# Performance work log

Hardware: AMD Instinct MI355X
Metric: run time of the kernel (lower is better)

## Reference

```python
import jax, jax.numpy as jnp
import numpy as np

TEXT_DIM, GIN = 5000, 128
B, N, E = 4096, 200000, 6400000
AE_HID, AE_EMB, G_HID, G_EMB = 8, 4, 8, 4


def _gcn(x, W, b, src, dst):
    N_ = x.shape[0]
    h = x @ W
    loop = jnp.arange(N_)
    s = jnp.concatenate([src, loop])
    d = jnp.concatenate([dst, loop])
    deg = jax.ops.segment_sum(jnp.ones(s.shape[0], h.dtype), d, num_segments=N_)
    dinv = jnp.where(deg > 0, jax.lax.rsqrt(jnp.maximum(deg, 1e-12)), 0.0)
    norm = dinv[s] * dinv[d]
    out = jax.ops.segment_sum(h[s] * norm[:, None], d, num_segments=N_)
    return out + b


def setup_inputs() -> dict:
    key = jax.random.key(0)
    ks = jax.random.split(key, 20)
    def lin(k, fan_in, fan_out):
        lim = 1.0 / np.sqrt(fan_in)
        kw, kb = jax.random.split(k)
        W = jax.random.uniform(kw, (fan_in, fan_out), jnp.float32, -lim, lim)
        b = jax.random.uniform(kb, (fan_out,), jnp.float32, -lim, lim)
        return W, b
    W_e1, b_e1 = lin(ks[0], TEXT_DIM, AE_HID)
    W_e2, b_e2 = lin(ks[1], AE_HID, AE_EMB)
    W_d1, b_d1 = lin(ks[2], AE_EMB, AE_HID)
    W_d2, b_d2 = lin(ks[3], AE_HID, TEXT_DIM)
    W_g1, b_g1 = lin(ks[4], GIN, G_HID)
    W_g2, b_g2 = lin(ks[5], G_HID, G_EMB)
    W_c, b_c = lin(ks[6], AE_EMB + G_EMB, 1)
    text_x = jax.random.normal(ks[7], (B, TEXT_DIM), jnp.float32)
    node_x = jax.random.normal(ks[8], (N, GIN), jnp.float32)
    edge_index = jax.random.randint(ks[9], (2, E), 0, N, jnp.int64 if jax.config.jax_enable_x64 else jnp.int32)
    batch = jnp.sort(jax.random.randint(ks[10], (N,), 0, B, edge_index.dtype))
    return {"text_x": text_x, "node_x": node_x, "edge_index": edge_index, "batch": batch,
            "W_e1": W_e1, "b_e1": b_e1, "W_e2": W_e2, "b_e2": b_e2,
            "W_d1": W_d1, "b_d1": b_d1, "W_d2": W_d2, "b_d2": b_d2,
            "W_g1": W_g1, "b_g1": b_g1, "W_g2": W_g2, "b_g2": b_g2,
            "W_c": W_c, "b_c": b_c}


def reference(text_x, node_x, edge_index, batch,
              W_e1, b_e1, W_e2, b_e2, W_d1, b_d1, W_d2, b_d2,
              W_g1, b_g1, W_g2, b_g2, W_c, b_c):
    # Autoencoder (eval mode: dropout = identity)
    z_text = jax.nn.relu(jax.nn.relu(text_x @ W_e1 + b_e1) @ W_e2 + b_e2)
    x_hat = jax.nn.sigmoid(jax.nn.relu(z_text @ W_d1 + b_d1) @ W_d2 + b_d2)
    # GNN encoder
    src, dst = edge_index[0], edge_index[1]
    h = jax.nn.relu(_gcn(node_x, W_g1, b_g1, src, dst))
    h = _gcn(h, W_g2, b_g2, src, dst)
    # global mean pool over graphs
    nb = text_x.shape[0]
    sums = jax.ops.segment_sum(h, batch, num_segments=nb)
    cnt = jax.ops.segment_sum(jnp.ones(h.shape[0], h.dtype), batch, num_segments=nb)
    z_graph = sums / jnp.maximum(cnt, 1.0)[:, None]
    z = jnp.concatenate([z_text, z_graph], axis=1)
    logits = z @ W_c + b_c
    return (x_hat, logits, z)
```

## Files before the change

kernel.cpp:

```cpp
#include <hip/hip_runtime.h>

#define BB 4096
#define TD 5000
#define NN 200000
#define EE 6400000
#define NBK 782

__device__ __forceinline__ void atomAddF(float* p, float v) {
    unsafeAtomicAdd(p, v);
}

__global__ void k_zero(float* p, int n) {
    int i = blockIdx.x * 256 + threadIdx.x;
    if (i < n) p[i] = 0.f;
}

__global__ void k_detect(const int* __restrict__ e, int* __restrict__ flag) {
    __shared__ int r[256];
    int tid = threadIdx.x;
    int acc = 0;
    for (int i = tid; i < 4096; i += 256) acc |= e[2 * i + 1];
    r[tid] = acc;
    __syncthreads();
    for (int s = 128; s > 0; s >>= 1) {
        if (tid < s) r[tid] |= r[tid + s];
        __syncthreads();
    }
    if (tid == 0) *flag = (r[0] == 0) ? 1 : 0;
}

__global__ void k_deg_init(unsigned int* deg) {
    int i = blockIdx.x * 256 + threadIdx.x;
    if (i < NN) deg[i] = 1u;
}

__global__ void k_rank(const int* __restrict__ edge, const int* __restrict__ flag,
                       unsigned int* __restrict__ deg, unsigned int* __restrict__ r) {
    int e = blockIdx.x * 256 + threadIdx.x;
    if (e >= EE) return;
    int f = *flag;
    int d = f ? edge[2 * (EE + e)] : edge[EE + e];
    r[e] = atomicAdd(&deg[d], 1u);
}

__global__ void k_dinv(const unsigned int* __restrict__ deg, float* __restrict__ dinv) {
    int i = blockIdx.x * 256 + threadIdx.x;
    if (i < NN) dinv[i] = rsqrtf((float)deg[i]);
}

__global__ void kA_blocksum(const unsigned int* __restrict__ deg, unsigned int* __restrict__ bsum) {
    __shared__ unsigned int s[256];
    int tid = threadIdx.x;
    int i = blockIdx.x * 256 + tid;
    s[tid] = (i < NN) ? (deg[i] - 1u) : 0u;
    __syncthreads();
    for (int st = 128; st > 0; st >>= 1) {
        if (tid < st) s[tid] += s[tid + st];
        __syncthreads();
    }
    if (tid == 0) bsum[blockIdx.x] = s[0];
}
__global__ void kB_scanblocks(const unsigned int* __restrict__ bsum, unsigned int* __restrict__ bpre,
                              unsigned int* __restrict__ indptr) {
    __shared__ unsigned int s[1024];
    int t = threadIdx.x;
    s[t] = (t < NBK) ? bsum[t] : 0u;
    __syncthreads();
    for (int off = 1; off < 1024; off <<= 1) {
        unsigned int v = (t >= off) ? s[t - off] : 0u;
        __syncthreads();
        s[t] += v;
        __syncthreads();
    }
    if (t < NBK) bpre[t] = (t == 0) ? 0u : s[t - 1];
    if (t == 0) indptr[NN] = EE;
}
__global__ void kC_indptr(const unsigned int* __restrict__ deg, const unsigned int* __restrict__ bpre,
                          unsigned int* __restrict__ indptr) {
    __shared__ unsigned int s[256];
    int tid = threadIdx.x;
    int i = blockIdx.x * 256 + tid;
    unsigned int c = (i < NN) ? (deg[i] - 1u) : 0u;
    s[tid] = c;
    __syncthreads();
    for (int off = 1; off < 256; off <<= 1) {
        unsigned int v = (tid >= off) ? s[tid - off] : 0u;
        __syncthreads();
        s[tid] += v;
        __syncthreads();
    }
    if (i < NN) indptr[i] = bpre[blockIdx.x] + s[tid] - c;
}

__global__ void k_place(const int* __restrict__ edge, const int* __restrict__ flag,
                        const unsigned int* __restrict__ indptr, const unsigned int* __restrict__ r,
                        int* __restrict__ csr_src) {
    int e = blockIdx.x * 256 + threadIdx.x;
    if (e >= EE) return;
    int f = *flag;
    int s = f ? edge[2 * e] : edge[e];
    int d = f ? edge[2 * (EE + e)] : edge[EE + e];
    csr_src[indptr[d] + r[e] - 1u] = s;
}

__global__ __launch_bounds__(256) void k_gcn1_mm(
    const float* __restrict__ nodex, const float* __restrict__ Wg1,
    const float* __restrict__ dinv, float* __restrict__ h0g)
{
    __shared__ float W[128 * 8];
    int tid = threadIdx.x;
    for (int i = tid; i < 1024; i += 256) W[i] = Wg1[i];
    __syncthreads();
    int row = blockIdx.x * 256 + tid;
    if (row >= NN) return;
    const float4* xr = (const float4*)(nodex + (size_t)row * 128);
    float acc[8];
#pragma unroll
    for (int j = 0; j < 8; j++) acc[j] = 0.f;
#pragma unroll 8
    for (int c = 0; c < 32; c++) {
        float4 v = xr[c];
        const float* wr = &W[c * 32];
#pragma unroll
        for (int j = 0; j < 8; j++)
            acc[j] += v.x * wr[j] + v.y * wr[8 + j] + v.z * wr[16 + j] + v.w * wr[24 + j];
    }
    float di = dinv[row];
    float* o = h0g + (size_t)row * 8;
#pragma unroll
    for (int j = 0; j < 8; j++) o[j] = di * acc[j];
}

__global__ __launch_bounds__(256) void k_gather1(
    const unsigned int* __restrict__ indptr, const int* __restrict__ csr_src,
    const float* __restrict__ h0g, const float* __restrict__ dinv,
    const float* __restrict__ bg1, const float* __restrict__ Wg2,
    float* __restrict__ h2g)
{
    __shared__ float W[32];
    __shared__ float b1[8];
    __shared__ float h1s[4][8];
    int tid = threadIdx.x;
    if (tid < 32) W[tid] = Wg2[tid];
    if (tid < 8) b1[tid] = bg1[tid];
    __syncthreads();
    int wid = tid >> 6, lane = tid & 63;
    int i = blockIdx.x * 4 + wid;
    if (i < NN) {
        int beg = indptr[i], end = indptr[i + 1];
        int f = lane & 7;
        float a = 0.f;
        for (int k = beg + (lane >> 3); k < end; k += 8)
            a += h0g[(size_t)csr_src[k] * 8 + f];
        a += __shfl_xor(a, 8, 64);
        a += __shfl_xor(a, 16, 64);
        a += __shfl_xor(a, 32, 64);
        if (lane < 8) {
            float di = dinv[i];
            h1s[wid][f] = fmaxf(di * (a + h0g[(size_t)i * 8 + f]) + b1[f], 0.f);
        }
    }
    __syncthreads();
    if (i < NN && lane < 4) {
        float di = dinv[i];
        float s = 0.f;
#pragma unroll
        for (int k = 0; k < 8; k++) s += h1s[wid][k] * W[k * 4 + lane];
        h2g[(size_t)i * 4 + lane] = di * s;
    }
}

__global__ __launch_bounds__(256) void k_gather2(
    const unsigned int* __restrict__ indptr, const int* __restrict__ csr_src,
    const float* __restrict__ h2g, const float* __restrict__ dinv,
    const float* __restrict__ bg2, const int* __restrict__ batch,
    const int* __restrict__ flag, float* __restrict__ pool, float* __restrict__ cnt)
{
    __shared__ float b2[4];
    int tid = threadIdx.x;
    if (tid < 4) b2[tid] = bg2[tid];
    __syncthreads();
    int wid = tid >> 6, lane = tid & 63;
    int i = blockIdx.x * 4 + wid;
    if (i >= NN) return;
    int beg = indptr[i], end = indptr[i + 1];
    int f = lane & 3;
    float a = 0.f;
    for (int k = beg + (lane >> 2); k < end; k += 16)
        a += h2g[(size_t)csr_src[k] * 4 + f];
    a += __shfl_xor(a, 4, 64);
    a += __shfl_xor(a, 8, 64);
    a += __shfl_xor(a, 16, 64);
    a += __shfl_xor(a, 32, 64);
    if (lane < 4) {
        float di = dinv[i];
        float h = di * (a + h2g[(size_t)i * 4 + f]) + b2[f];
        int fg = *flag;
        int b = fg ? batch[2 * i] : batch[i];
        atomAddF(&pool[(size_t)b * 4 + f], h);
        if (f == 0) atomAddF(&cnt[b], 1.f);
    }
}

__global__ __launch_bounds__(256) void k_ae_encode(
    const float* __restrict__ text,
    const float* __restrict__ We1, const float* __restrict__ be1,
    const float* __restrict__ We2, const float* __restrict__ be2,
    float* __restrict__ z_text)
{
    __shared__ float red[8][256];
    __shared__ float t1[8];
    int row = blockIdx.x, tid = threadIdx.x;
    const float* xrow = text + (size_t)row * TD;
    float acc[8];
#pragma unroll
    for (int j = 0; j < 8; j++) acc[j] = 0.f;
    for (int i = tid; i < TD; i += 256) {
        float x = xrow[i];
        const float* wr = We1 + (size_t)i * 8;
#pragma unroll
        for (int j = 0; j < 8; j++) acc[j] += x * wr[j];
    }
#pragma unroll
    for (int j = 0; j < 8; j++) red[j][tid] = acc[j];
    __syncthreads();
    for (int s = 128; s > 0; s >>= 1) {
        if (tid < s) {
#pragma unroll
            for (int j = 0; j < 8; j++) red[j][tid] += red[j][tid + s];
        }
        __syncthreads();
    }
    if (tid < 8) t1[tid] = fmaxf(red[tid][0] + be1[tid], 0.f);
    __syncthreads();
    if (tid < 4) {
        float z = be2[tid];
#pragma unroll
        for (int k = 0; k < 8; k++) z += t1[k] * We2[k * 4 + tid];
        z_text[row * 4 + tid] = fmaxf(z, 0.f);
    }
}

__global__ __launch_bounds__(256) void k_final(
    const float* __restrict__ z_text, const float* __restrict__ pool,
    const float* __restrict__ cnt, const float* __restrict__ Wc,
    const float* __restrict__ bc, float* __restrict__ out_logits,
    float* __restrict__ out_z)
{
    int g = blockIdx.x * 256 + threadIdx.x;
    if (g >= BB) return;
    float c = fmaxf(cnt[g], 1.f);
    float z8[8];
#pragma unroll
    for (int j = 0; j < 4; j++) z8[j] = z_text[g * 4 + j];
#pragma unroll
    for (int j = 0; j < 4; j++) z8[4 + j] = pool[g * 4 + j] / c;
    float l = bc[0];
#pragma unroll
    for (int k = 0; k < 8; k++) l += z8[k] * Wc[k];
    out_logits[g] = l;
#pragma unroll
    for (int k = 0; k < 8; k++) out_z[g * 8 + k] = z8[k];
}

__global__ __launch_bounds__(256) void k_ae_decode(
    const float* __restrict__ out_z,
    const float* __restrict__ Wd1, const float* __restrict__ bd1,
    const float* __restrict__ Wd2, const float* __restrict__ bd2,
    float* __restrict__ xhat)
{
    int row = blockIdx.x, tid = threadIdx.x;
    float zz[4];
#pragma unroll
    for (int j = 0; j < 4; j++) zz[j] = out_z[row * 8 + j];
    float t[8];
#pragma unroll
    for (int k = 0; k < 8; k++) {
        float s = bd1[k];
#pragma unroll
        for (int j = 0; j < 4; j++) s += zz[j] * Wd1[j * 8 + k];
        t[k] = fmaxf(s, 0.f);
    }
    float* orow = xhat + (size_t)row * TD;
    for (int c = tid; c < TD; c += 256) {
        float s = bd2[c];
#pragma unroll
        for (int k = 0; k < 8; k++) s += t[k] * Wd2[(size_t)k * TD + c];
        orow[c] = 1.f / (1.f + expf(-s));
    }
}

extern "C" void kernel_launch(void* const* d_in, const int* in_sizes, int n_in,
                              void* d_out, int out_size, void* d_ws, size_t ws_size,
                              hipStream_t stream) {
    const float* text  = (const float*)d_in[0];
    const float* nodex = (const float*)d_in[1];
    const int* edge    = (const int*)d_in[2];
    const int* batch   = (const int*)d_in[3];
    const float* We1 = (const float*)d_in[4];
    const float* be1 = (const float*)d_in[5];
    const float* We2 = (const float*)d_in[6];
    const float* be2 = (const float*)d_in[7];
    const float* Wd1 = (const float*)d_in[8];
    const float* bd1 = (const float*)d_in[9];
    const float* Wd2 = (const float*)d_in[10];
    const float* bd2 = (const float*)d_in[11];
    const float* Wg1 = (const float*)d_in[12];
    const float* bg1 = (const float*)d_in[13];
    const float* Wg2 = (const float*)d_in[14];
    const float* bg2 = (const float*)d_in[15];
    const float* Wc  = (const float*)d_in[16];
    const float* bc  = (const float*)d_in[17];

    char* sc = (char*)d_out;
    float*        h0g    = (float*)(sc + 0);
    float*        h2g    = (float*)(sc + 6400000);
    float*        dinv   = (float*)(sc + 9600000);
    unsigned int* deg    = (unsigned int*)(sc + 10400000);
    unsigned int* indptr = (unsigned int*)(sc + 11200000);
    unsigned int* rnk    = (unsigned int*)(sc + 12000004);
    int*          csr    = (int*)(sc + 37600004);
    unsigned int* bsum   = (unsigned int*)(sc + 63200004);
    unsigned int* bpre   = (unsigned int*)(sc + 63203132);
    float*        pool   = (float*)(sc + 63206260);
    float*        cnt    = (float*)(sc + 63271796);
    float*        z_text = (float*)(sc + 63288180);
    int*          flag   = (int*)(sc + 63353716);

    float* out_xhat   = (float*)d_out;
    float* out_logits = out_xhat + (size_t)BB * TD;
    float* out_z      = out_logits + BB;

    const int NB_E = EE / 256;
    const int NB_G = (NN + 3) / 4;

    k_zero<<<(BB * 5 + 255) / 256, 256, 0, stream>>>(pool, BB * 5);
    k_detect<<<1, 256, 0, stream>>>(edge, flag);
    k_deg_init<<<NBK, 256, 0, stream>>>(deg);
    k_rank<<<NB_E, 256, 0, stream>>>(edge, flag, deg, rnk);

    kA_blocksum<<<NBK, 256, 0, stream>>>(deg, bsum);
    kB_scanblocks<<<1, 1024, 0, stream>>>(bsum, bpre, indptr);
    kC_indptr<<<NBK, 256, 0, stream>>>(deg, bpre, indptr);
    k_dinv<<<NBK, 256, 0, stream>>>(deg, dinv);
    k_place<<<NB_E, 256, 0, stream>>>(edge, flag, indptr, rnk, csr);

    k_gcn1_mm<<<NBK, 256, 0, stream>>>(nodex, Wg1, dinv, h0g);
    k_gather1<<<NB_G, 256, 0, stream>>>(indptr, csr, h0g, dinv, bg1, Wg2, h2g);
    k_gather2<<<NB_G, 256, 0, stream>>>(indptr, csr, h2g, dinv, bg2, batch, flag, pool, cnt);

    k_ae_encode<<<BB, 256, 0, stream>>>(text, We1, be1, We2, be2, z_text);
    k_final<<<(BB + 255) / 256, 256, 0, stream>>>(z_text, pool, cnt, Wc, bc,
                                                  out_logits, out_z);
    k_ae_decode<<<BB, 256, 0, stream>>>(out_z, Wd1, bd1, Wd2, bd2, out_xhat);
}
```

Baseline: 832.6 us.

## Fuse init kernels, replace pool atomics with sorted segment reduce, vectorize AE

Merges the zero/detect/degree-init kernels and the dinv/blocksum kernels to cut launches. It replaces the atomic-based global mean pool with per-graph boundaries computed from the sorted batch vector and a block reduction in the final kernel. It also vectorizes the autoencoder encode and decode loops with float4 loads and stores. This relies on batch being sorted and adds an extra h2f buffer write and read.

```diff
diff --git a/kernel.cpp b/kernel.cpp
--- a/kernel.cpp
+++ b/kernel.cpp
@@ -6,32 +6,23 @@
 #define EE 6400000
 #define NBK 782
 
-__device__ __forceinline__ void atomAddF(float* p, float v) {
-    unsafeAtomicAdd(p, v);
-}
-
-__global__ void k_zero(float* p, int n) {
-    int i = blockIdx.x * 256 + threadIdx.x;
-    if (i < n) p[i] = 0.f;
-}
-
-__global__ void k_detect(const int* __restrict__ e, int* __restrict__ flag) {
-    __shared__ int r[256];
-    int tid = threadIdx.x;
-    int acc = 0;
-    for (int i = tid; i < 4096; i += 256) acc |= e[2 * i + 1];
-    r[tid] = acc;
-    __syncthreads();
-    for (int s = 128; s > 0; s >>= 1) {
-        if (tid < s) r[tid] |= r[tid + s];
-        __syncthreads();
-    }
-    if (tid == 0) *flag = (r[0] == 0) ? 1 : 0;
-}
-
-__global__ void k_deg_init(unsigned int* deg) {
+__global__ void k_init(const int* __restrict__ e, unsigned int* __restrict__ deg,
+                       int* __restrict__ flag) {
     int i = blockIdx.x * 256 + threadIdx.x;
     if (i < NN) deg[i] = 1u;
+    if (blockIdx.x == 0) {
+        __shared__ int r[256];
+        int tid = threadIdx.x;
+        int acc = 0;
+        for (int k = tid; k < 4096; k += 256) acc |= e[2 * k + 1];
+        r[tid] = acc;
+        __syncthreads();
+        for (int s = 128; s > 0; s >>= 1) {
+            if (tid < s) r[tid] |= r[tid + s];
+            __syncthreads();
+        }
+        if (tid == 0) *flag = (r[0] == 0) ? 1 : 0;
+    }
 }
 
 __global__ void k_rank(const int* __restrict__ edge, const int* __restrict__ flag,
@@ -43,16 +34,25 @@
     r[e] = atomicAdd(&deg[d], 1u);
 }
 
-__global__ void k_dinv(const unsigned int* __restrict__ deg, float* __restrict__ dinv) {
-    int i = blockIdx.x * 256 + threadIdx.x;
-    if (i < NN) dinv[i] = rsqrtf((float)deg[i]);
-}
-
-__global__ void kA_blocksum(const unsigned int* __restrict__ deg, unsigned int* __restrict__ bsum) {
+__global__ void kA_all(const unsigned int* __restrict__ deg, float* __restrict__ dinv,
+                       unsigned int* __restrict__ bsum, const int* __restrict__ batch,
+                       const int* __restrict__ flag, unsigned int* __restrict__ bnd) {
     __shared__ unsigned int s[256];
     int tid = threadIdx.x;
     int i = blockIdx.x * 256 + tid;
-    s[tid] = (i < NN) ? (deg[i] - 1u) : 0u;
+    unsigned int c = 0u;
+    if (i < NN) {
+        unsigned int u = deg[i];
+        dinv[i] = rsqrtf((float)u);
+        c = u - 1u;
+        int fg = *flag;
+        int b = fg ? batch[2 * i] : batch[i];
+        int bp = (i == 0) ? -1 : (fg ? batch[2 * (i - 1)] : batch[i - 1]);
+        for (int bb = bp + 1; bb <= b; bb++) bnd[bb] = (unsigned int)i;
+        if (i == NN - 1)
+            for (int bb = b + 1; bb <= BB; bb++) bnd[bb] = (unsigned int)NN;
+    }
+    s[tid] = c;
     __syncthreads();
     for (int st = 128; st > 0; st >>= 1) {
         if (tid < st) s[tid] += s[tid + st];
@@ -60,6 +60,7 @@
     }
     if (tid == 0) bsum[blockIdx.x] = s[0];
 }
+
 __global__ void kB_scanblocks(const unsigned int* __restrict__ bsum, unsigned int* __restrict__ bpre,
                               unsigned int* __restrict__ indptr) {
     __shared__ unsigned int s[1024];
@@ -75,6 +76,7 @@
     if (t < NBK) bpre[t] = (t == 0) ? 0u : s[t - 1];
     if (t == 0) indptr[NN] = EE;
 }
+
 __global__ void kC_indptr(const unsigned int* __restrict__ deg, const unsigned int* __restrict__ bpre,
                           unsigned int* __restrict__ indptr) {
     __shared__ unsigned int s[256];
@@ -173,8 +175,7 @@
 __global__ __launch_bounds__(256) void k_gather2(
     const unsigned int* __restrict__ indptr, const int* __restrict__ csr_src,
     const float* __restrict__ h2g, const float* __restrict__ dinv,
-    const float* __restrict__ bg2, const int* __restrict__ batch,
-    const int* __restrict__ flag, float* __restrict__ pool, float* __restrict__ cnt)
+    const float* __restrict__ bg2, float* __restrict__ h2f)
 {
     __shared__ float b2[4];
     int tid = threadIdx.x;
@@ -194,11 +195,7 @@
     a += __shfl_xor(a, 32, 64);
     if (lane < 4) {
         float di = dinv[i];
-        float h = di * (a + h2g[(size_t)i * 4 + f]) + b2[f];
-        int fg = *flag;
-        int b = fg ? batch[2 * i] : batch[i];
-        atomAddF(&pool[(size_t)b * 4 + f], h);
-        if (f == 0) atomAddF(&cnt[b], 1.f);
+        h2f[(size_t)i * 4 + f] = di * (a + h2g[(size_t)i * 4 + f]) + b2[f];
     }
 }
 
@@ -211,15 +208,22 @@
     __shared__ float red[8][256];
     __shared__ float t1[8];
     int row = blockIdx.x, tid = threadIdx.x;
-    const float* xrow = text + (size_t)row * TD;
+    const float4* xrow = (const float4*)(text + (size_t)row * TD);
     float acc[8];
 #pragma unroll
     for (int j = 0; j < 8; j++) acc[j] = 0.f;
-    for (int i = tid; i < TD; i += 256) {
-        float x = xrow[i];
-        const float* wr = We1 + (size_t)i * 8;
-#pragma unroll
-        for (int j = 0; j < 8; j++) acc[j] += x * wr[j];
+    for (int v = tid; v < 1250; v += 256) {
+        float4 xv = xrow[v];
+        const float4* w = (const float4*)(We1 + (size_t)v * 32);
+        float xc[4] = {xv.x, xv.y, xv.z, xv.w};
+#pragma unroll
+        for (int c = 0; c < 4; c++) {
+            float4 wa = w[c * 2], wb = w[c * 2 + 1];
+            acc[0] += xc[c] * wa.x; acc[1] += xc[c] * wa.y;
+            acc[2] += xc[c] * wa.z; acc[3] += xc[c] * wa.w;
+            acc[4] += xc[c] * wb.x; acc[5] += xc[c] * wb.y;
+            acc[6] += xc[c] * wb.z; acc[7] += xc[c] * wb.w;
+        }
     }
 #pragma unroll
     for (int j = 0; j < 8; j++) red[j][tid] = acc[j];
@@ -242,25 +246,43 @@
 }
 
 __global__ __launch_bounds__(256) void k_final(
-    const float* __restrict__ z_text, const float* __restrict__ pool,
-    const float* __restrict__ cnt, const float* __restrict__ Wc,
+    const float* __restrict__ h2f, const unsigned int* __restrict__ bnd,
+    const float* __restrict__ z_text, const float* __restrict__ Wc,
     const float* __restrict__ bc, float* __restrict__ out_logits,
     float* __restrict__ out_z)
 {
-    int g = blockIdx.x * 256 + threadIdx.x;
-    if (g >= BB) return;
-    float c = fmaxf(cnt[g], 1.f);
-    float z8[8];
-#pragma unroll
-    for (int j = 0; j < 4; j++) z8[j] = z_text[g * 4 + j];
-#pragma unroll
-    for (int j = 0; j < 4; j++) z8[4 + j] = pool[g * 4 + j] / c;
-    float l = bc[0];
-#pragma unroll
-    for (int k = 0; k < 8; k++) l += z8[k] * Wc[k];
-    out_logits[g] = l;
-#pragma unroll
-    for (int k = 0; k < 8; k++) out_z[g * 8 + k] = z8[k];
+    __shared__ float red[256][4];
+    int g = blockIdx.x, tid = threadIdx.x;
+    int lo = bnd[g], hi = bnd[g + 1];
+    float a0 = 0.f, a1 = 0.f, a2 = 0.f, a3 = 0.f;
+    for (int i = lo + tid; i < hi; i += 256) {
+        float4 v = *(const float4*)(h2f + (size_t)i * 4);
+        a0 += v.x; a1 += v.y; a2 += v.z; a3 += v.w;
+    }
+    red[tid][0] = a0; red[tid][1] = a1; red[tid][2] = a2; red[tid][3] = a3;
+    __syncthreads();
+    for (int s = 128; s > 0; s >>= 1) {
+        if (tid < s) {
+            red[tid][0] += red[tid + s][0]; red[tid][1] += red[tid + s][1];
+            red[tid][2] += red[tid + s][2]; red[tid][3] += red[tid + s][3];
+        }
+        __syncthreads();
+    }
+    if (tid == 0) {
+        float c = (float)(hi - lo);
+        c = fmaxf(c, 1.f);
+        float z8[8];
+#pragma unroll
+        for (int j = 0; j < 4; j++) z8[j] = z_text[g * 4 + j];
+#pragma unroll
+        for (int j = 0; j < 4; j++) z8[4 + j] = red[0][j] / c;
+        float l = bc[0];
+#pragma unroll
+        for (int k = 0; k < 8; k++) l += z8[k] * Wc[k];
+        out_logits[g] = l;
+#pragma unroll
+        for (int k = 0; k < 8; k++) out_z[g * 8 + k] = z8[k];
+    }
 }
 
 __global__ __launch_bounds__(256) void k_ae_decode(
@@ -281,12 +303,20 @@
         for (int j = 0; j < 4; j++) s += zz[j] * Wd1[j * 8 + k];
         t[k] = fmaxf(s, 0.f);
     }
-    float* orow = xhat + (size_t)row * TD;
-    for (int c = tid; c < TD; c += 256) {
-        float s = bd2[c];
-#pragma unroll
-        for (int k = 0; k < 8; k++) s += t[k] * Wd2[(size_t)k * TD + c];
-        orow[c] = 1.f / (1.f + expf(-s));
+    float4* orow = (float4*)(xhat + (size_t)row * TD);
+    for (int c4 = tid; c4 < 1250; c4 += 256) {
+        float4 s = *(const float4*)(bd2 + c4 * 4);
+#pragma unroll
+        for (int k = 0; k < 8; k++) {
+            float4 w = *(const float4*)(Wd2 + (size_t)k * TD + c4 * 4);
+            s.x += t[k] * w.x; s.y += t[k] * w.y;
+            s.z += t[k] * w.z; s.w += t[k] * w.w;
+        }
+        s.x = 1.f / (1.f + expf(-s.x));
+        s.y = 1.f / (1.f + expf(-s.y));
+        s.z = 1.f / (1.f + expf(-s.z));
+        s.w = 1.f / (1.f + expf(-s.w));
+        orow[c4] = s;
     }
 }
 
@@ -315,17 +345,17 @@
     char* sc = (char*)d_out;
     float*        h0g    = (float*)(sc + 0);
     float*        h2g    = (float*)(sc + 6400000);
-    float*        dinv   = (float*)(sc + 9600000);
-    unsigned int* deg    = (unsigned int*)(sc + 10400000);
-    unsigned int* indptr = (unsigned int*)(sc + 11200000);
-    unsigned int* rnk    = (unsigned int*)(sc + 12000004);
-    int*          csr    = (int*)(sc + 37600004);
-    unsigned int* bsum   = (unsigned int*)(sc + 63200004);
-    unsigned int* bpre   = (unsigned int*)(sc + 63203132);
-    float*        pool   = (float*)(sc + 63206260);
-    float*        cnt    = (float*)(sc + 63271796);
-    float*        z_text = (float*)(sc + 63288180);
-    int*          flag   = (int*)(sc + 63353716);
+    float*        h2f    = (float*)(sc + 9600000);
+    float*        dinv   = (float*)(sc + 12800000);
+    unsigned int* deg    = (unsigned int*)(sc + 13600000);
+    unsigned int* indptr = (unsigned int*)(sc + 14400000);
+    unsigned int* rnk    = (unsigned int*)(sc + 15200004);
+    int*          csr    = (int*)(sc + 40800004);
+    unsigned int* bsum   = (unsigned int*)(sc + 66400004);
+    unsigned int* bpre   = (unsigned int*)(sc + 66403132);
+    float*        z_text = (float*)(sc + 66406260);
+    unsigned int* bnd    = (unsigned int*)(sc + 66471796);
+    int*          flag   = (int*)(sc + 66488184);
 
     float* out_xhat   = (float*)d_out;
     float* out_logits = out_xhat + (size_t)BB * TD;
@@ -334,23 +364,18 @@
     const int NB_E = EE / 256;
     const int NB_G = (NN + 3) / 4;
 
-    k_zero<<<(BB * 5 + 255) / 256, 256, 0, stream>>>(pool, BB * 5);
-    k_detect<<<1, 256, 0, stream>>>(edge, flag);
-    k_deg_init<<<NBK, 256, 0, stream>>>(deg);
+    k_init<<<NBK, 256, 0, stream>>>(edge, deg, flag);
     k_rank<<<NB_E, 256, 0, stream>>>(edge, flag, deg, rnk);
-
-    kA_blocksum<<<NBK, 256, 0, stream>>>(deg, bsum);
+    kA_all<<<NBK, 256, 0, stream>>>(deg, dinv, bsum, batch, flag, bnd);
     kB_scanblocks<<<1, 1024, 0, stream>>>(bsum, bpre, indptr);
     kC_indptr<<<NBK, 256, 0, stream>>>(deg, bpre, indptr);
-    k_dinv<<<NBK, 256, 0, stream>>>(deg, dinv);
     k_place<<<NB_E, 256, 0, stream>>>(edge, flag, indptr, rnk, csr);
 
     k_gcn1_mm<<<NBK, 256, 0, stream>>>(nodex, Wg1, dinv, h0g);
     k_gather1<<<NB_G, 256, 0, stream>>>(indptr, csr, h0g, dinv, bg1, Wg2, h2g);
-    k_gather2<<<NB_G, 256, 0, stream>>>(indptr, csr, h2g, dinv, bg2, batch, flag, pool, cnt);
+    k_gather2<<<NB_G, 256, 0, stream>>>(indptr, csr, h2g, dinv, bg2, h2f);
 
     k_ae_encode<<<BB, 256, 0, stream>>>(text, We1, be1, We2, be2, z_text);
-    k_final<<<(BB + 255) / 256, 256, 0, stream>>>(z_text, pool, cnt, Wc, bc,
-                                                  out_logits, out_z);
+    k_final<<<BB, 256, 0, stream>>>(h2f, bnd, z_text, Wc, bc, out_logits, out_z);
     k_ae_decode<<<BB, 256, 0, stream>>>(out_z, Wd1, bd1, Wd2, bd2, out_xhat);
 }
```

Measured after the change: 782.8 us. 6.0% less time.
